# Kernel tuning notes

Hardware: AMD Instinct MI355X
Metric: run time of the kernel (lower is better)

The kernel has to match this reference:

```python
import jax, jax.numpy as jnp
import numpy as np

B, T, C, H = 4, 2048, 768, 64

def setup_inputs() -> dict:
    key = jax.random.key(0)
    k1, k2, k3, k4 = jax.random.split(key, 4)
    x = jax.random.normal(k1, (B, T, C), dtype=jnp.float32)
    # Dense kernels (glorot-ish scale)
    s = 1.0 / np.sqrt(C)
    Wq = jax.random.normal(k2, (C, H), dtype=jnp.float32) * s
    Wk = jax.random.normal(k3, (C, H), dtype=jnp.float32) * s
    Wv = jax.random.normal(k4, (C, H), dtype=jnp.float32) * s
    return {"x": x, "Wq": Wq, "Wk": Wk, "Wv": Wv}

def reference(x, Wq, Wk, Wv):
    # q, k, v: [B, T, H]
    q = jnp.einsum('btc,ch->bth', x, Wq)
    k = jnp.einsum('btc,ch->bth', x, Wk)
    v = jnp.einsum('btc,ch->bth', x, Wv)
    scale = k.shape[-1] ** -0.5
    # scores: [B, T, T]
    scores = jnp.einsum('bth,bsh->bts', q, k) * scale
    # causal mask: lower-triangular allowed
    causal = jnp.tril(jnp.ones((T, T), dtype=bool))
    scores = jnp.where(causal, scores, -jnp.inf)
    weights = jax.nn.softmax(scores, axis=-1)
    # dropout is inactive at inference (Keras default training=False)
    out = jnp.einsum('bts,bsh->bth', weights, v)
    return out
```

## Files before the change

kernel.cpp:

```cpp
#include <hip/hip_runtime.h>
#include <hip/hip_bf16.h>
#include <math.h>

constexpr int BB = 4;
constexpr int TT = 2048;
constexpr int CC = 768;
constexpr int HH = 64;
constexpr int NSPLIT = 8;

#define QSCALE 0.1803368801111204f

typedef __attribute__((ext_vector_type(8))) short bf16x8;
typedef __attribute__((ext_vector_type(4))) float f32x4;

__device__ inline ushort f2bf(float f) {
    uint u = __float_as_uint(f);
    u += 0x7fffu + ((u >> 16) & 1u);
    return (ushort)(u >> 16);
}

__device__ inline float fexp2(float x) { return __builtin_amdgcn_exp2f(x); }

__device__ inline bf16x8 cvt8(const float4 a, const float4 b) {
    union { bf16x8 v; __hip_bfloat162 h[4]; } u;
    u.h[0] = __float22bfloat162_rn(make_float2(a.x, a.y));
    u.h[1] = __float22bfloat162_rn(make_float2(a.z, a.w));
    u.h[2] = __float22bfloat162_rn(make_float2(b.x, b.y));
    u.h[3] = __float22bfloat162_rn(make_float2(b.z, b.w));
    return u.v;
}

__global__ __launch_bounds__(256) void prep_w(const float* __restrict__ Wq,
                                              const float* __restrict__ Wk,
                                              const float* __restrict__ Wv,
                                              ushort* __restrict__ Wt) {
    const int k0  = blockIdx.x * 64;
    const int mat = blockIdx.y;
    const float* W = (mat == 0) ? Wq : (mat == 1) ? Wk : Wv;
    __shared__ ushort tile[64 * 66];
    const int tid = threadIdx.x;

    for (int i = tid; i < 1024; i += 256) {
        int kk = i >> 4, c = i & 15;
        float4 f = ((const float4*)W)[(k0 + kk) * 16 + c];
        ushort* d = &tile[kk * 66 + c * 4];
        d[0] = f2bf(f.x); d[1] = f2bf(f.y); d[2] = f2bf(f.z); d[3] = f2bf(f.w);
    }
    __syncthreads();
    for (int i = tid; i < 512; i += 256) {
        int n = i >> 3, c8 = i & 7;
        bf16x8 v;
        #pragma unroll
        for (int j = 0; j < 8; ++j)
            ((ushort*)&v)[j] = tile[(c8 * 8 + j) * 66 + n];
        *(bf16x8*)&Wt[(size_t)(mat * 64 + n) * CC + k0 + c8 * 8] = v;
    }
}

__global__ __launch_bounds__(256) void qkv_mfma(const float* __restrict__ x,
                                                const ushort* __restrict__ Wt,
                                                ushort* __restrict__ qg,
                                                ushort* __restrict__ kg,
                                                ushort* __restrict__ vtg) {
    __shared__ ushort xs[2][32 * 72];
    __shared__ ushort ws[2][192 * 72];
    __shared__ ushort vts[64 * 40];
    const int tid  = threadIdx.x;
    const int row0 = blockIdx.x * 32;
    const int lane = tid & 63, w = tid >> 6;
    const int l15  = lane & 15, quad = lane >> 4;
    const int m0   = (w & 1) * 16;
    const int cg   = (w >> 1) * 96;

    f32x4 acc[6];
    #pragma unroll
    for (int i = 0; i < 6; ++i) acc[i] = (f32x4){0.f, 0.f, 0.f, 0.f};

    const int ar = tid >> 3, ac = tid & 7;
    const float* xg = x + (size_t)(row0 + ar) * CC + ac * 8;

    {
        const float4* xp = (const float4*)xg;
        *(bf16x8*)&xs[0][ar * 72 + ac * 8] = cvt8(xp[0], xp[1]);
        #pragma unroll
        for (int j = 0; j < 6; ++j) {
            int c = tid + j * 256;
            int rw = c >> 3, cc = c & 7;
            *(bf16x8*)&ws[0][rw * 72 + cc * 8] =
                *(const bf16x8*)&Wt[(size_t)rw * CC + cc * 8];
        }
    }
    __syncthreads();

    for (int kc = 0; kc < 12; ++kc) {
        const int cur = kc & 1, nxt = cur ^ 1;
        const bool have = (kc + 1 < 12);

        float4 f0, f1;
        bf16x8 wreg[6];
        if (have) {
            const float4* xp = (const float4*)(xg + (kc + 1) * 64);
            f0 = xp[0]; f1 = xp[1];
            #pragma unroll
            for (int j = 0; j < 6; ++j) {
                int c = tid + j * 256;
                int rw = c >> 3, cc = c & 7;
                wreg[j] = *(const bf16x8*)&Wt[(size_t)rw * CC + (kc + 1) * 64 + cc * 8];
            }
        }

        #pragma unroll
        for (int ks = 0; ks < 2; ++ks) {
            bf16x8 a = *(const bf16x8*)&xs[cur][(m0 + l15) * 72 + ks * 32 + quad * 8];
            #pragma unroll
            for (int nt = 0; nt < 6; ++nt) {
                bf16x8 bfr = *(const bf16x8*)
                    &ws[cur][(cg + nt * 16 + l15) * 72 + ks * 32 + quad * 8];
                acc[nt] = __builtin_amdgcn_mfma_f32_16x16x32_bf16(a, bfr, acc[nt], 0, 0, 0);
            }
        }

        if (have) {
            *(bf16x8*)&xs[nxt][ar * 72 + ac * 8] = cvt8(f0, f1);
            #pragma unroll
            for (int j = 0; j < 6; ++j) {
                int c = tid + j * 256;
                int rw = c >> 3, cc = c & 7;
                *(bf16x8*)&ws[nxt][rw * 72 + cc * 8] = wreg[j];
            }
        }
        __syncthreads();
    }

    #pragma unroll
    for (int nt = 0; nt < 6; ++nt) {
        int n = cg + nt * 16 + l15;
        #pragma unroll
        for (int r = 0; r < 4; ++r) {
            int row = row0 + m0 + quad * 4 + r;
            float vacc = acc[nt][r];
            if (n < 64)       qg[(size_t)row * HH + n] = f2bf(vacc * QSCALE);
            else if (n < 128) kg[(size_t)row * HH + (n - 64)] = f2bf(vacc);
            else              vts[(n - 128) * 40 + (m0 + quad * 4 + r)] = f2bf(vacc);
        }
    }
    __syncthreads();
    {
        int h = tid >> 2, p = tid & 3;
        int b = row0 >> 11, tl = row0 & 2047;
        bf16x8 v = *(const bf16x8*)&vts[h * 40 + p * 8];
        *(bf16x8*)&vtg[(size_t)b * (HH * TT) + (size_t)h * TT + tl + p * 8] = v;
    }
}

__global__ __launch_bounds__(128) void attn_split(const ushort* __restrict__ qg,
                                                  const ushort* __restrict__ kg,
                                                  const ushort* __restrict__ vtg,
                                                  float* __restrict__ Op,
                                                  float* __restrict__ ml) {
    const int qt2 = blockIdx.x, b = blockIdx.y, split = blockIdx.z;
    const int tid  = threadIdx.x;
    const int lane = tid & 63, w = tid >> 6;
    const int l15  = lane & 15, quad = lane >> 4;
    const int t0   = qt2 * 32;
    const int pidx = ((b * 64 + qt2) << 3) + split;

    const int ntile = (qt2 >> 1) + 1;
    const int lo = (ntile * split) >> 3;
    const int hi = (ntile * (split + 1)) >> 3;

    if (lo >= hi) {
        float4 z = (float4){0.f, 0.f, 0.f, 0.f};
        float4* op4 = (float4*)(Op + (size_t)pidx * 2048);
        #pragma unroll
        for (int j = 0; j < 4; ++j) op4[tid * 4 + j] = z;
        if (tid < 32) {
            ml[pidx * 64 + tid]      = -1e30f;
            ml[pidx * 64 + 32 + tid] = 0.f;
        }
        return;
    }

    __shared__ ushort Ps[2][16 * 72];

    const ushort* qp = &qg[(size_t)(b * TT + t0 + w * 16 + l15) * HH + quad * 8];
    bf16x8 qa0 = *(const bf16x8*)qp;
    bf16x8 qa1 = *(const bf16x8*)(qp + 32);

    const ushort* kbb = &kg[(size_t)(b * TT + l15) * HH + quad * 8];
    const ushort* vbb = &vtg[(size_t)b * (HH * TT) + (size_t)l15 * TT + quad * 8];

    f32x4 po[4];
    #pragma unroll
    for (int i = 0; i < 4; ++i) po[i] = (f32x4){0.f, 0.f, 0.f, 0.f};
    float mrun[4] = {-1e30f, -1e30f, -1e30f, -1e30f};
    float lrun[4] = {0.f, 0.f, 0.f, 0.f};

    bf16x8 kb[8], vb[8];
    #pragma unroll
    for (int nt = 0; nt < 4; ++nt) {
        const ushort* kp = kbb + (size_t)(lo * 64 + nt * 16) * HH;
        kb[2 * nt]     = *(const bf16x8*)kp;
        kb[2 * nt + 1] = *(const bf16x8*)(kp + 32);
    }

    for (int st = lo; st < hi; ++st) {
        f32x4 sf[4];
        #pragma unroll
        for (int nt = 0; nt < 4; ++nt) {
            f32x4 z = (f32x4){0.f, 0.f, 0.f, 0.f};
            z = __builtin_amdgcn_mfma_f32_16x16x32_bf16(qa0, kb[2 * nt], z, 0, 0, 0);
            sf[nt] = __builtin_amdgcn_mfma_f32_16x16x32_bf16(qa1, kb[2 * nt + 1], z, 0, 0, 0);
        }
        if (st + 1 < hi) {
            #pragma unroll
            for (int nt = 0; nt < 4; ++nt) {
                const ushort* kp = kbb + (size_t)((st + 1) * 64 + nt * 16) * HH;
                kb[2 * nt]     = *(const bf16x8*)kp;
                kb[2 * nt + 1] = *(const bf16x8*)(kp + 32);
            }
        }
        #pragma unroll
        for (int jj = 0; jj < 4; ++jj) {
            const ushort* vp = vbb + (size_t)(jj * 16) * TT + st * 64;
            vb[2 * jj]     = *(const bf16x8*)vp;
            vb[2 * jj + 1] = *(const bf16x8*)(vp + 32);
        }

        float p[4][4];
        float rm[4] = {-1e30f, -1e30f, -1e30f, -1e30f};
        if (st == ntile - 1) {
            #pragma unroll
            for (int nt = 0; nt < 4; ++nt) {
                int s_abs = st * 64 + nt * 16 + l15;
                #pragma unroll
                for (int r = 0; r < 4; ++r) {
                    int t_abs = t0 + w * 16 + quad * 4 + r;
                    float v = (s_abs > t_abs) ? -1e30f : sf[nt][r];
                    p[nt][r] = v;
                    rm[r] = fmaxf(rm[r], v);
                }
            }
        } else {
            #pragma unroll
            for (int nt = 0; nt < 4; ++nt)
                #pragma unroll
                for (int r = 0; r < 4; ++r) {
                    p[nt][r] = sf[nt][r];
                    rm[r] = fmaxf(rm[r], sf[nt][r]);
                }
        }
        float alpha[4], rs[4] = {0.f, 0.f, 0.f, 0.f};
        #pragma unroll
        for (int r = 0; r < 4; ++r) {
            float v = rm[r];
            v = fmaxf(v, __shfl_xor(v, 1, 64));
            v = fmaxf(v, __shfl_xor(v, 2, 64));
            v = fmaxf(v, __shfl_xor(v, 4, 64));
            v = fmaxf(v, __shfl_xor(v, 8, 64));
            float mnew = fmaxf(mrun[r], v);
            alpha[r] = fexp2(mrun[r] - mnew);
            mrun[r] = mnew;
        }
        #pragma unroll
        for (int nt = 0; nt < 4; ++nt)
            #pragma unroll
            for (int r = 0; r < 4; ++r) {
                float e = fexp2(p[nt][r] - mrun[r]);
                p[nt][r] = e;
                rs[r] += e;
            }
        #pragma unroll
        for (int r = 0; r < 4; ++r) {
            float v = rs[r];
            v += __shfl_xor(v, 1, 64);
            v += __shfl_xor(v, 2, 64);
            v += __shfl_xor(v, 4, 64);
            v += __shfl_xor(v, 8, 64);
            lrun[r] = lrun[r] * alpha[r] + v;
        }
        #pragma unroll
        for (int jj = 0; jj < 4; ++jj)
            #pragma unroll
            for (int r = 0; r < 4; ++r)
                po[jj][r] *= alpha[r];

        #pragma unroll
        for (int nt = 0; nt < 4; ++nt)
            #pragma unroll
            for (int r = 0; r < 4; ++r)
                Ps[w][(quad * 4 + r) * 72 + nt * 16 + l15] = f2bf(p[nt][r]);
        bf16x8 pa0 = *(const bf16x8*)&Ps[w][l15 * 72 + quad * 8];
        bf16x8 pa1 = *(const bf16x8*)&Ps[w][l15 * 72 + 32 + quad * 8];

        #pragma unroll
        for (int jj = 0; jj < 4; ++jj) {
            po[jj] = __builtin_amdgcn_mfma_f32_16x16x32_bf16(pa0, vb[2 * jj], po[jj], 0, 0, 0);
            po[jj] = __builtin_amdgcn_mfma_f32_16x16x32_bf16(pa1, vb[2 * jj + 1], po[jj], 0, 0, 0);
        }
    }

    #pragma unroll
    for (int jj = 0; jj < 4; ++jj)
        #pragma unroll
        for (int r = 0; r < 4; ++r)
            Op[(size_t)pidx * 2048 + (w * 16 + quad * 4 + r) * 64 + jj * 16 + l15] =
                po[jj][r];
    if (l15 == 0) {
        #pragma unroll
        for (int r = 0; r < 4; ++r) {
            int row = w * 16 + quad * 4 + r;
            ml[pidx * 64 + row]      = mrun[r];
            ml[pidx * 64 + 32 + row] = lrun[r];
        }
    }
}

__global__ __launch_bounds__(256) void attn_merge(const float* __restrict__ Op,
                                                  const float* __restrict__ ml,
                                                  float* __restrict__ out) {
    const int tid = threadIdx.x;
    const int w = tid >> 6, lane = tid & 63;
    const int row = blockIdx.x * 4 + w;
    const int b = row >> 11, t = row & 2047;
    const int qt2 = t >> 5, rl = t & 31;
    const int pbase = ((b * 64 + qt2) << 3);

    float m[NSPLIT], l[NSPLIT];
    #pragma unroll
    for (int i = 0; i < NSPLIT; ++i) {
        m[i] = ml[(pbase + i) * 64 + rl];
        l[i] = ml[(pbase + i) * 64 + 32 + rl];
    }
    float M = -1e30f;
    #pragma unroll
    for (int i = 0; i < NSPLIT; ++i) M = fmaxf(M, m[i]);
    float wgt[NSPLIT], L = 0.f;
    #pragma unroll
    for (int i = 0; i < NSPLIT; ++i) {
        wgt[i] = fexp2(m[i] - M);
        L += wgt[i] * l[i];
    }
    float acc = 0.f;
    #pragma unroll
    for (int i = 0; i < NSPLIT; ++i)
        acc += wgt[i] * Op[(size_t)(pbase + i) * 2048 + rl * 64 + lane];
    out[(size_t)row * HH + lane] = acc / L;
}

extern "C" void kernel_launch(void* const* d_in, const int* in_sizes, int n_in,
                              void* d_out, int out_size, void* d_ws, size_t ws_size,
                              hipStream_t stream)
{
    const float* x  = (const float*)d_in[0];
    const float* Wq = (const float*)d_in[1];
    const float* Wk = (const float*)d_in[2];
    const float* Wv = (const float*)d_in[3];
    float* out = (float*)d_out;

    ushort* qg  = (ushort*)d_ws;
    ushort* kg  = qg  + (size_t)BB * TT * HH;
    ushort* vtg = kg  + (size_t)BB * TT * HH;
    ushort* Wt  = vtg + (size_t)BB * TT * HH;
    float*  Op  = (float*)(Wt + (size_t)3 * HH * CC);
    float*  ml  = Op + (size_t)2048 * 2048;

    prep_w    <<<dim3(12, 3),           dim3(256), 0, stream>>>(Wq, Wk, Wv, Wt);
    qkv_mfma  <<<dim3((BB * TT) / 32),  dim3(256), 0, stream>>>(x, Wt, qg, kg, vtg);
    attn_split<<<dim3(64, BB, NSPLIT),  dim3(128), 0, stream>>>(qg, kg, vtg, Op, ml);
    attn_merge<<<dim3((BB * TT) / 4),   dim3(256), 0, stream>>>(Op, ml, out);
}
```

Before: 118.8 us.

## Fuse split-KV attention and merge into one block with LDS reduction

Replaces the separate split-attention and merge kernels with a single 512-thread block per 32-query tile. Each of four wave pairs handles one KV split, and the partial outputs and row max/sum values are merged through shared memory. This removes the global partial-output buffer round trip and one kernel launch. In exchange it halves the split count, giving 256 blocks of 8 waves instead of 2048 small blocks, and uses a large amount of LDS per block. Both changes may reduce parallelism and hurt load balance on long causal rows.

```diff
diff --git a/kernel.cpp b/kernel.cpp
--- a/kernel.cpp
+++ b/kernel.cpp
@@ -6,7 +6,7 @@
 constexpr int TT = 2048;
 constexpr int CC = 768;
 constexpr int HH = 64;
-constexpr int NSPLIT = 8;
+constexpr int NSPLIT = 4;
 
 #define QSCALE 0.1803368801111204f
 
@@ -153,199 +153,185 @@
     }
 }
 
-__global__ __launch_bounds__(128) void attn_split(const ushort* __restrict__ qg,
+__global__ __launch_bounds__(512) void attn_block(const ushort* __restrict__ qg,
                                                   const ushort* __restrict__ kg,
                                                   const ushort* __restrict__ vtg,
-                                                  float* __restrict__ Op,
-                                                  float* __restrict__ ml) {
-    const int qt2 = blockIdx.x, b = blockIdx.y, split = blockIdx.z;
+                                                  float* __restrict__ out) {
+    const int qt2 = blockIdx.x, b = blockIdx.y;
     const int tid  = threadIdx.x;
     const int lane = tid & 63, w = tid >> 6;
+    const int split = w >> 1, ws2 = w & 1;
     const int l15  = lane & 15, quad = lane >> 4;
     const int t0   = qt2 * 32;
-    const int pidx = ((b * 64 + qt2) << 3) + split;
 
     const int ntile = (qt2 >> 1) + 1;
-    const int lo = (ntile * split) >> 3;
-    const int hi = (ntile * (split + 1)) >> 3;
+    const int lo = (ntile * split) >> 2;
+    const int hi = (ntile * (split + 1)) >> 2;
+
+    __shared__ ushort Ps[8][16 * 72];
+    __shared__ float  Opart[NSPLIT][32 * 64];
+    __shared__ float  mlm[NSPLIT][32];
+    __shared__ float  mll[NSPLIT][32];
 
     if (lo >= hi) {
-        float4 z = (float4){0.f, 0.f, 0.f, 0.f};
-        float4* op4 = (float4*)(Op + (size_t)pidx * 2048);
-        #pragma unroll
-        for (int j = 0; j < 4; ++j) op4[tid * 4 + j] = z;
-        if (tid < 32) {
-            ml[pidx * 64 + tid]      = -1e30f;
-            ml[pidx * 64 + 32 + tid] = 0.f;
-        }
-        return;
-    }
-
-    __shared__ ushort Ps[2][16 * 72];
-
-    const ushort* qp = &qg[(size_t)(b * TT + t0 + w * 16 + l15) * HH + quad * 8];
-    bf16x8 qa0 = *(const bf16x8*)qp;
-    bf16x8 qa1 = *(const bf16x8*)(qp + 32);
-
-    const ushort* kbb = &kg[(size_t)(b * TT + l15) * HH + quad * 8];
-    const ushort* vbb = &vtg[(size_t)b * (HH * TT) + (size_t)l15 * TT + quad * 8];
-
-    f32x4 po[4];
+        if (ws2 == 0 && lane < 32) {
+            mlm[split][lane] = -1e30f;
+            mll[split][lane] = 0.f;
+        }
+    } else {
+        const ushort* qp = &qg[(size_t)(b * TT + t0 + ws2 * 16 + l15) * HH + quad * 8];
+        bf16x8 qa0 = *(const bf16x8*)qp;
+        bf16x8 qa1 = *(const bf16x8*)(qp + 32);
+
+        const ushort* kbb = &kg[(size_t)(b * TT + l15) * HH + quad * 8];
+        const ushort* vbb = &vtg[(size_t)b * (HH * TT) + (size_t)l15 * TT + quad * 8];
+
+        f32x4 po[4];
+        #pragma unroll
+        for (int i = 0; i < 4; ++i) po[i] = (f32x4){0.f, 0.f, 0.f, 0.f};
+        float mrun[4] = {-1e30f, -1e30f, -1e30f, -1e30f};
+        float lrun[4] = {0.f, 0.f, 0.f, 0.f};
+
+        bf16x8 kb[8], vb[8];
+        #pragma unroll
+        for (int nt = 0; nt < 4; ++nt) {
+            const ushort* kp = kbb + (size_t)(lo * 64 + nt * 16) * HH;
+            kb[2 * nt]     = *(const bf16x8*)kp;
+            kb[2 * nt + 1] = *(const bf16x8*)(kp + 32);
+        }
+
+        for (int st = lo; st < hi; ++st) {
+            f32x4 sf[4];
+            #pragma unroll
+            for (int nt = 0; nt < 4; ++nt) {
+                f32x4 z = (f32x4){0.f, 0.f, 0.f, 0.f};
+                z = __builtin_amdgcn_mfma_f32_16x16x32_bf16(qa0, kb[2 * nt], z, 0, 0, 0);
+                sf[nt] = __builtin_amdgcn_mfma_f32_16x16x32_bf16(qa1, kb[2 * nt + 1], z, 0, 0, 0);
+            }
+            if (st + 1 < hi) {
+                #pragma unroll
+                for (int nt = 0; nt < 4; ++nt) {
+                    const ushort* kp = kbb + (size_t)((st + 1) * 64 + nt * 16) * HH;
+                    kb[2 * nt]     = *(const bf16x8*)kp;
+                    kb[2 * nt + 1] = *(const bf16x8*)(kp + 32);
+                }
+            }
+            #pragma unroll
+            for (int jj = 0; jj < 4; ++jj) {
+                const ushort* vp = vbb + (size_t)(jj * 16) * TT + st * 64;
+                vb[2 * jj]     = *(const bf16x8*)vp;
+                vb[2 * jj + 1] = *(const bf16x8*)(vp + 32);
+            }
+
+            float p[4][4];
+            float rm[4] = {-1e30f, -1e30f, -1e30f, -1e30f};
+            if (st == ntile - 1) {
+                #pragma unroll
+                for (int nt = 0; nt < 4; ++nt) {
+                    int s_abs = st * 64 + nt * 16 + l15;
+                    #pragma unroll
+                    for (int r = 0; r < 4; ++r) {
+                        int t_abs = t0 + ws2 * 16 + quad * 4 + r;
+                        float v = (s_abs > t_abs) ? -1e30f : sf[nt][r];
+                        p[nt][r] = v;
+                        rm[r] = fmaxf(rm[r], v);
+                    }
+                }
+            } else {
+                #pragma unroll
+                for (int nt = 0; nt < 4; ++nt)
+                    #pragma unroll
+                    for (int r = 0; r < 4; ++r) {
+                        p[nt][r] = sf[nt][r];
+                        rm[r] = fmaxf(rm[r], sf[nt][r]);
+                    }
+            }
+            float alpha[4], rs[4] = {0.f, 0.f, 0.f, 0.f};
+            #pragma unroll
+            for (int r = 0; r < 4; ++r) {
+                float v = rm[r];
+                v = fmaxf(v, __shfl_xor(v, 1, 64));
+                v = fmaxf(v, __shfl_xor(v, 2, 64));
+                v = fmaxf(v, __shfl_xor(v, 4, 64));
+                v = fmaxf(v, __shfl_xor(v, 8, 64));
+                float mnew = fmaxf(mrun[r], v);
+                alpha[r] = fexp2(mrun[r] - mnew);
+                mrun[r] = mnew;
+            }
+            #pragma unroll
+            for (int nt = 0; nt < 4; ++nt)
+                #pragma unroll
+                for (int r = 0; r < 4; ++r) {
+                    float e = fexp2(p[nt][r] - mrun[r]);
+                    p[nt][r] = e;
+                    rs[r] += e;
+                }
+            #pragma unroll
+            for (int r = 0; r < 4; ++r) {
+                float v = rs[r];
+                v += __shfl_xor(v, 1, 64);
+                v += __shfl_xor(v, 2, 64);
+                v += __shfl_xor(v, 4, 64);
+                v += __shfl_xor(v, 8, 64);
+                lrun[r] = lrun[r] * alpha[r] + v;
+            }
+            #pragma unroll
+            for (int jj = 0; jj < 4; ++jj)
+                #pragma unroll
+                for (int r = 0; r < 4; ++r)
+                    po[jj][r] *= alpha[r];
+
+            #pragma unroll
+            for (int nt = 0; nt < 4; ++nt)
+                #pragma unroll
+                for (int r = 0; r < 4; ++r)
+                    Ps[w][(quad * 4 + r) * 72 + nt * 16 + l15] = f2bf(p[nt][r]);
+            bf16x8 pa0 = *(const bf16x8*)&Ps[w][l15 * 72 + quad * 8];
+            bf16x8 pa1 = *(const bf16x8*)&Ps[w][l15 * 72 + 32 + quad * 8];
+
+            #pragma unroll
+            for (int jj = 0; jj < 4; ++jj) {
+                po[jj] = __builtin_amdgcn_mfma_f32_16x16x32_bf16(pa0, vb[2 * jj], po[jj], 0, 0, 0);
+                po[jj] = __builtin_amdgcn_mfma_f32_16x16x32_bf16(pa1, vb[2 * jj + 1], po[jj], 0, 0, 0);
+            }
+        }
+
+        #pragma unroll
+        for (int jj = 0; jj < 4; ++jj)
+            #pragma unroll
+            for (int r = 0; r < 4; ++r)
+                Opart[split][(ws2 * 16 + quad * 4 + r) * 64 + jj * 16 + l15] = po[jj][r];
+        if (l15 == 0) {
+            #pragma unroll
+            for (int r = 0; r < 4; ++r) {
+                int row = ws2 * 16 + quad * 4 + r;
+                mlm[split][row] = mrun[r];
+                mll[split][row] = lrun[r];
+            }
+        }
+    }
+
+    __syncthreads();
+
     #pragma unroll
-    for (int i = 0; i < 4; ++i) po[i] = (f32x4){0.f, 0.f, 0.f, 0.f};
-    float mrun[4] = {-1e30f, -1e30f, -1e30f, -1e30f};
-    float lrun[4] = {0.f, 0.f, 0.f, 0.f};
-
-    bf16x8 kb[8], vb[8];
-    #pragma unroll
-    for (int nt = 0; nt < 4; ++nt) {
-        const ushort* kp = kbb + (size_t)(lo * 64 + nt * 16) * HH;
-        kb[2 * nt]     = *(const bf16x8*)kp;
-        kb[2 * nt + 1] = *(const bf16x8*)(kp + 32);
-    }
-
-    for (int st = lo; st < hi; ++st) {
-        f32x4 sf[4];
-        #pragma unroll
-        for (int nt = 0; nt < 4; ++nt) {
-            f32x4 z = (f32x4){0.f, 0.f, 0.f, 0.f};
-            z = __builtin_amdgcn_mfma_f32_16x16x32_bf16(qa0, kb[2 * nt], z, 0, 0, 0);
-            sf[nt] = __builtin_amdgcn_mfma_f32_16x16x32_bf16(qa1, kb[2 * nt + 1], z, 0, 0, 0);
-        }
-        if (st + 1 < hi) {
-            #pragma unroll
-            for (int nt = 0; nt < 4; ++nt) {
-                const ushort* kp = kbb + (size_t)((st + 1) * 64 + nt * 16) * HH;
-                kb[2 * nt]     = *(const bf16x8*)kp;
-                kb[2 * nt + 1] = *(const bf16x8*)(kp + 32);
-            }
-        }
-        #pragma unroll
-        for (int jj = 0; jj < 4; ++jj) {
-            const ushort* vp = vbb + (size_t)(jj * 16) * TT + st * 64;
-            vb[2 * jj]     = *(const bf16x8*)vp;
-            vb[2 * jj + 1] = *(const bf16x8*)(vp + 32);
-        }
-
-        float p[4][4];
-        float rm[4] = {-1e30f, -1e30f, -1e30f, -1e30f};
-        if (st == ntile - 1) {
-            #pragma unroll
-            for (int nt = 0; nt < 4; ++nt) {
-                int s_abs = st * 64 + nt * 16 + l15;
-                #pragma unroll
-                for (int r = 0; r < 4; ++r) {
-                    int t_abs = t0 + w * 16 + quad * 4 + r;
-                    float v = (s_abs > t_abs) ? -1e30f : sf[nt][r];
-                    p[nt][r] = v;
-                    rm[r] = fmaxf(rm[r], v);
-                }
-            }
-        } else {
-            #pragma unroll
-            for (int nt = 0; nt < 4; ++nt)
-                #pragma unroll
-                for (int r = 0; r < 4; ++r) {
-                    p[nt][r] = sf[nt][r];
-                    rm[r] = fmaxf(rm[r], sf[nt][r]);
-                }
-        }
-        float alpha[4], rs[4] = {0.f, 0.f, 0.f, 0.f};
-        #pragma unroll
-        for (int r = 0; r < 4; ++r) {
-            float v = rm[r];
-            v = fmaxf(v, __shfl_xor(v, 1, 64));
-            v = fmaxf(v, __shfl_xor(v, 2, 64));
-            v = fmaxf(v, __shfl_xor(v, 4, 64));
-            v = fmaxf(v, __shfl_xor(v, 8, 64));
-            float mnew = fmaxf(mrun[r], v);
-            alpha[r] = fexp2(mrun[r] - mnew);
-            mrun[r] = mnew;
-        }
-        #pragma unroll
-        for (int nt = 0; nt < 4; ++nt)
-            #pragma unroll
-            for (int r = 0; r < 4; ++r) {
-                float e = fexp2(p[nt][r] - mrun[r]);
-                p[nt][r] = e;
-                rs[r] += e;
-            }
-        #pragma unroll
-        for (int r = 0; r < 4; ++r) {
-            float v = rs[r];
-            v += __shfl_xor(v, 1, 64);
-            v += __shfl_xor(v, 2, 64);
-            v += __shfl_xor(v, 4, 64);
-            v += __shfl_xor(v, 8, 64);
-            lrun[r] = lrun[r] * alpha[r] + v;
-        }
-        #pragma unroll
-        for (int jj = 0; jj < 4; ++jj)
-            #pragma unroll
-            for (int r = 0; r < 4; ++r)
-                po[jj][r] *= alpha[r];
-
-        #pragma unroll
-        for (int nt = 0; nt < 4; ++nt)
-            #pragma unroll
-            for (int r = 0; r < 4; ++r)
-                Ps[w][(quad * 4 + r) * 72 + nt * 16 + l15] = f2bf(p[nt][r]);
-        bf16x8 pa0 = *(const bf16x8*)&Ps[w][l15 * 72 + quad * 8];
-        bf16x8 pa1 = *(const bf16x8*)&Ps[w][l15 * 72 + 32 + quad * 8];
-
-        #pragma unroll
-        for (int jj = 0; jj < 4; ++jj) {
-            po[jj] = __builtin_amdgcn_mfma_f32_16x16x32_bf16(pa0, vb[2 * jj], po[jj], 0, 0, 0);
-            po[jj] = __builtin_amdgcn_mfma_f32_16x16x32_bf16(pa1, vb[2 * jj + 1], po[jj], 0, 0, 0);
-        }
-    }
-
-    #pragma unroll
-    for (int jj = 0; jj < 4; ++jj)
-        #pragma unroll
-        for (int r = 0; r < 4; ++r)
-            Op[(size_t)pidx * 2048 + (w * 16 + quad * 4 + r) * 64 + jj * 16 + l15] =
-                po[jj][r];
-    if (l15 == 0) {
-        #pragma unroll
-        for (int r = 0; r < 4; ++r) {
-            int row = w * 16 + quad * 4 + r;
-            ml[pidx * 64 + row]      = mrun[r];
-            ml[pidx * 64 + 32 + row] = lrun[r];
-        }
-    }
-}
-
-__global__ __launch_bounds__(256) void attn_merge(const float* __restrict__ Op,
-                                                  const float* __restrict__ ml,
-                                                  float* __restrict__ out) {
-    const int tid = threadIdx.x;
-    const int w = tid >> 6, lane = tid & 63;
-    const int row = blockIdx.x * 4 + w;
-    const int b = row >> 11, t = row & 2047;
-    const int qt2 = t >> 5, rl = t & 31;
-    const int pbase = ((b * 64 + qt2) << 3);
-
-    float m[NSPLIT], l[NSPLIT];
-    #pragma unroll
-    for (int i = 0; i < NSPLIT; ++i) {
-        m[i] = ml[(pbase + i) * 64 + rl];
-        l[i] = ml[(pbase + i) * 64 + 32 + rl];
-    }
-    float M = -1e30f;
-    #pragma unroll
-    for (int i = 0; i < NSPLIT; ++i) M = fmaxf(M, m[i]);
-    float wgt[NSPLIT], L = 0.f;
-    #pragma unroll
-    for (int i = 0; i < NSPLIT; ++i) {
-        wgt[i] = fexp2(m[i] - M);
-        L += wgt[i] * l[i];
-    }
-    float acc = 0.f;
-    #pragma unroll
-    for (int i = 0; i < NSPLIT; ++i)
-        acc += wgt[i] * Op[(size_t)(pbase + i) * 2048 + rl * 64 + lane];
-    out[(size_t)row * HH + lane] = acc / L;
+    for (int j = 0; j < 4; ++j) {
+        int e  = tid + j * 512;
+        int rr = e >> 6, h = e & 63;
+        float M = -1e30f;
+        #pragma unroll
+        for (int i = 0; i < NSPLIT; ++i) M = fmaxf(M, mlm[i][rr]);
+        float L = 0.f, acc = 0.f;
+        #pragma unroll
+        for (int i = 0; i < NSPLIT; ++i) {
+            float li = mll[i][rr];
+            if (li > 0.f) {
+                float wgt = fexp2(mlm[i][rr] - M);
+                L   += wgt * li;
+                acc += wgt * Opart[i][rr * 64 + h];
+            }
+        }
+        out[(size_t)(b * TT + t0 + rr) * HH + h] = acc / L;
+    }
 }
 
 extern "C" void kernel_launch(void* const* d_in, const int* in_sizes, int n_in,
@@ -362,11 +348,8 @@
     ushort* kg  = qg  + (size_t)BB * TT * HH;
     ushort* vtg = kg  + (size_t)BB * TT * HH;
     ushort* Wt  = vtg + (size_t)BB * TT * HH;
-    float*  Op  = (float*)(Wt + (size_t)3 * HH * CC);
-    float*  ml  = Op + (size_t)2048 * 2048;
-
-    prep_w    <<<dim3(12, 3),           dim3(256), 0, stream>>>(Wq, Wk, Wv, Wt);
-    qkv_mfma  <<<dim3((BB * TT) / 32),  dim3(256), 0, stream>>>(x, Wt, qg, kg, vtg);
-    attn_split<<<dim3(64, BB, NSPLIT),  dim3(128), 0, stream>>>(qg, kg, vtg, Op, ml);
-    attn_merge<<<dim3((BB * TT) / 4),   dim3(256), 0, stream>>>(Op, ml, out);
-}
+
+    prep_w    <<<dim3(12, 3),          dim3(256), 0, stream>>>(Wq, Wk, Wv, Wt);
+    qkv_mfma  <<<dim3((BB * TT) / 32), dim3(256), 0, stream>>>(x, Wt, qg, kg, vtg);
+    attn_block<<<dim3(64, BB),         dim3(512), 0, stream>>>(qg, kg, vtg, out);
+}
```

New measurement: 115.6 us. 2.8% less time.
